# Kernel optimization log

Hardware: AMD Instinct MI355X
Metric: run time of the kernel (lower is better)

Reference implementation:

```python
import jax, jax.numpy as jnp
import numpy as np

INPUT_SIZE = 512
HIDDEN_SIZE = 256
B, S = 8, 2048


def setup_inputs() -> dict:
    key = jax.random.key(0)
    ks = jax.random.split(key, 9)
    d = INPUT_SIZE
    q = jax.random.normal(ks[0], (B, S, 2 * HIDDEN_SIZE), dtype=jnp.float32)
    k = jax.random.normal(ks[1], (B, S, d), dtype=jnp.float32)
    v = jax.random.normal(ks[2], (B, S, d), dtype=jnp.float32)
    # Params: module uses nn.init.normal_ (std=1); keep normal but scale for stability.
    Wq = jax.random.normal(ks[3], (2 * HIDDEN_SIZE, d), dtype=jnp.float32) * 0.02
    bq = jax.random.normal(ks[4], (d,), dtype=jnp.float32) * 0.02
    Wk = jax.random.normal(ks[5], (d, d), dtype=jnp.float32) * 0.02
    bk = jax.random.normal(ks[6], (d,), dtype=jnp.float32) * 0.02
    Wv = jax.random.normal(ks[7], (d, d), dtype=jnp.float32) * 0.02
    bv = jax.random.normal(ks[8], (d,), dtype=jnp.float32) * 0.02
    return {"q": q, "k": k, "v": v, "Wq": Wq, "bq": bq, "Wk": Wk, "bk": bk, "Wv": Wv, "bv": bv}


def reference(q, k, v, Wq, bq, Wk, bk, Wv, bv):
    d = Wq.shape[-1]
    qp = jnp.einsum('bsh,hd->bsd', q, Wq) + bq  # [B,S,d]
    kp = jnp.einsum('bse,ed->bsd', k, Wk) + bk
    vp = jnp.einsum('bse,ed->bsd', v, Wv) + bv
    scale = 1.0 / jnp.sqrt(jnp.float32(d))
    scores = jnp.einsum('bqd,bkd->bqk', qp, kp) * scale  # [B,S,S]
    attn = jax.nn.softmax(scores, axis=-1)
    return jnp.einsum('bqk,bkd->bqd', attn, vp)
```

## Files before the change

### kernel.cpp

```cpp
#include <hip/hip_runtime.h>
#include <hip/hip_bf16.h>
#include <stdint.h>


typedef __attribute__((ext_vector_type(8))) short short8;
typedef __attribute__((ext_vector_type(4))) float floatx4;

__device__ __forceinline__ unsigned short f2bf(float f) {
    union { float f; uint32_t u; } v; v.f = f;
    uint32_t u = v.u;
    return (unsigned short)((u + 0x7FFF + ((u >> 16) & 1)) >> 16);
}

#define ASYNC16(g, l)                                                          \
    __builtin_amdgcn_global_load_lds(                                          \
        (const __attribute__((address_space(1))) unsigned int*)(g),            \
        (__attribute__((address_space(3))) unsigned int*)(l), 16, 0, 0)

__global__ void wt_kernel(const float* __restrict__ Wq, const float* __restrict__ Wk,
                          const float* __restrict__ Wv, unsigned short* __restrict__ WT) {
    __shared__ float t[64][65];
    const int z = blockIdx.z;
    const float* W = (z == 0) ? Wq : ((z == 1) ? Wk : Wv);
    const int n0 = blockIdx.x * 64, k0 = blockIdx.y * 64;
    const int tx = threadIdx.x & 63, ty = threadIdx.x >> 6;
#pragma unroll
    for (int i = ty; i < 64; i += 4) t[i][tx] = W[(size_t)(k0 + i) * 512 + n0 + tx];
    __syncthreads();
#pragma unroll
    for (int i = ty; i < 64; i += 4)
        WT[(size_t)z * 262144 + (size_t)(n0 + i) * 512 + k0 + tx] = f2bf(t[tx][i]);
}

__global__ __launch_bounds__(256, 4) void proj_kernel(
    const float* __restrict__ q, const float* __restrict__ k, const float* __restrict__ v,
    const float* __restrict__ bq, const float* __restrict__ bk, const float* __restrict__ bv,
    const unsigned short* __restrict__ WT,
    unsigned short* __restrict__ qp, unsigned short* __restrict__ kp,
    unsigned short* __restrict__ vpT)
{
    __shared__ __align__(16) unsigned short At[2][64][32];
    __shared__ __align__(16) unsigned short Bt[2][256][32];

    const int z = blockIdx.z;
    const int tid = threadIdx.x;
    const int lane = tid & 63;
    const int wave = tid >> 6;
    const int col = lane & 15;
    const int quad = lane >> 4;

    const float* A = (z == 0) ? q : ((z == 1) ? k : v);
    const float* bias = (z == 0) ? bq : ((z == 1) ? bk : bv);
    const unsigned short* W = WT + (size_t)z * 262144;

    const int m0 = blockIdx.x * 64;
    const int n0b = blockIdx.y * 256;

    floatx4 acc[4][4];
#pragma unroll
    for (int mf = 0; mf < 4; ++mf)
#pragma unroll
        for (int nf = 0; nf < 4; ++nf) acc[mf][nf] = floatx4{0.f, 0.f, 0.f, 0.f};

    auto stageB = [&](int nb, int kc) {
#pragma unroll
        for (int j = 0; j < 4; ++j) {
            const int rr = (wave * 4 + j) * 16 + (lane >> 2);
            const unsigned short* g =
                W + (size_t)(n0b + rr) * 512 + kc * 32 + (((lane & 3) ^ ((rr >> 1) & 3)) << 3);
            ASYNC16(g, &Bt[nb][(wave * 4 + j) * 16][0]);
        }
    };

    float4 fA0, fA1;
    const int arow = tid >> 2;
    auto loadA = [&](int kc) {
        const float* ap = A + (size_t)(m0 + arow) * 512 + kc * 32 + (tid & 3) * 8;
        fA0 = *(const float4*)ap;
        fA1 = *(const float4*)(ap + 4);
    };
    auto writeA = [&](int nb) {
        short8 t;
        t[0] = f2bf(fA0.x); t[1] = f2bf(fA0.y); t[2] = f2bf(fA0.z); t[3] = f2bf(fA0.w);
        t[4] = f2bf(fA1.x); t[5] = f2bf(fA1.y); t[6] = f2bf(fA1.z); t[7] = f2bf(fA1.w);
        *(short8*)&At[nb][arow][(((tid & 3) ^ ((arow >> 1) & 3)) << 3)] = t;
    };

    stageB(0, 0);
    loadA(0);
    writeA(0);
    for (int kc = 0; kc < 16; ++kc) {
        const int cur = kc & 1;
        __syncthreads();
        if (kc < 15) { stageB(cur ^ 1, kc + 1); loadA(kc + 1); }

        const int rsw = (quad ^ ((col >> 1) & 3)) << 3;
        short8 a[4], bfr[4];
#pragma unroll
        for (int mf = 0; mf < 4; ++mf)
            a[mf] = *(const short8*)&At[cur][mf * 16 + col][rsw];
#pragma unroll
        for (int nf = 0; nf < 4; ++nf)
            bfr[nf] = *(const short8*)&Bt[cur][wave * 64 + nf * 16 + col][rsw];
#pragma unroll
        for (int mf = 0; mf < 4; ++mf)
#pragma unroll
            for (int nf = 0; nf < 4; ++nf)
                acc[mf][nf] = __builtin_amdgcn_mfma_f32_16x16x32_bf16(a[mf], bfr[nf], acc[mf][nf], 0, 0, 0);

        if (kc < 15) writeA(cur ^ 1);
    }

    const float scale = (z == 0) ? 0.04419417382415922f : 1.0f;
#pragma unroll
    for (int mf = 0; mf < 4; ++mf) {
#pragma unroll
        for (int nf = 0; nf < 4; ++nf) {
            const int n = n0b + wave * 64 + nf * 16 + col;
            const float bn2 = bias[n];
            floatx4 c = acc[mf][nf];
            if (z < 2) {
                unsigned short* outp = (z == 0) ? qp : kp;
#pragma unroll
                for (int r = 0; r < 4; ++r) {
                    int row = m0 + mf * 16 + quad * 4 + r;
                    outp[(size_t)row * 512 + n] = f2bf((c[r] + bn2) * scale);
                }
            } else {
                int row = m0 + mf * 16 + quad * 4;
                int bb = row >> 11;
                int s = row & 2047;
                ushort4 pk;
                pk.x = f2bf(c[0] + bn2); pk.y = f2bf(c[1] + bn2);
                pk.z = f2bf(c[2] + bn2); pk.w = f2bf(c[3] + bn2);
                *(ushort4*)(vpT + (((size_t)bb * 64 + (s >> 5)) * 512 + n) * 32 + (s & 31)) = pk;
            }
        }
    }
}

__global__ __launch_bounds__(512, 2) void attn_kernel(
    const unsigned short* __restrict__ qp, const unsigned short* __restrict__ kp,
    const unsigned short* __restrict__ vpT, float* __restrict__ out,
    float* __restrict__ Opart, float* __restrict__ lws)
{
    __shared__ __align__(16) unsigned short Kt[2][32][512];
    __shared__ __align__(16) unsigned short Vt[2][512][32];
    __shared__ __align__(16) unsigned short Pbuf[8][16][40];

    const int lane = threadIdx.x & 63;
    const int wave = threadIdx.x >> 6;
    const int col = lane & 15;
    const int quad = lane >> 4;
    const int b = blockIdx.x & 7;
    const int qt = (blockIdx.x >> 3) & 15;
    const int ksp = blockIdx.x >> 7;
    const int q0 = qt * 128 + wave * 16;
    const size_t rowbase = (size_t)b * 2048 + q0;

    const unsigned short* kpb = kp + (size_t)b * 2048 * 512;
    const unsigned short* vpb = vpT + ((size_t)b << 20);

    short8 aq[16];
#pragma unroll
    for (int kk = 0; kk < 16; ++kk)
        aq[kk] = *(const short8*)(qp + (rowbase + col) * 512 + kk * 32 + quad * 8);

    floatx4 o[32];
#pragma unroll
    for (int i = 0; i < 32; ++i) o[i] = floatx4{0.f, 0.f, 0.f, 0.f};
    float plsum[4] = {0.f, 0.f, 0.f, 0.f};

    auto stage = [&](int nb, int keyblk) {
#pragma unroll
        for (int j = 0; j < 4; ++j) {
            const int r = wave * 4 + j;
            const unsigned short* g =
                kpb + ((size_t)(keyblk * 32 + r) << 9) + ((lane ^ (r & 7)) << 3);
            ASYNC16(g, &Kt[nb][r][0]);
        }
        const unsigned short* vtile = vpb + ((size_t)keyblk << 14);
#pragma unroll
        for (int jj = 0; jj < 4; ++jj) {
            const int j2 = wave * 4 + jj;
            const int d = j2 * 16 + (lane >> 2);
            const unsigned short* g =
                vtile + ((size_t)d << 5) + (((lane & 3) ^ ((d >> 1) & 3)) << 3);
            ASYNC16(g, &Vt[nb][j2 * 16][0]);
        }
    };

    stage(0, ksp * 32);
    for (int kb = 0; kb < 32; ++kb) {
        const int cur = kb & 1;
        __syncthreads();
        if (kb < 31) stage(cur ^ 1, ksp * 32 + kb + 1);

        floatx4 s0 = floatx4{0.f, 0.f, 0.f, 0.f};
        floatx4 s1 = floatx4{0.f, 0.f, 0.f, 0.f};
        __builtin_amdgcn_s_setprio(1);
#pragma unroll
        for (int kk = 0; kk < 16; ++kk) {
            const int c = (kk << 2) + quad;
            short8 b0 = *(const short8*)&Kt[cur][col][(c ^ (col & 7)) << 3];
            short8 b1 = *(const short8*)&Kt[cur][16 + col][(c ^ (col & 7)) << 3];
            s0 = __builtin_amdgcn_mfma_f32_16x16x32_bf16(aq[kk], b0, s0, 0, 0, 0);
            s1 = __builtin_amdgcn_mfma_f32_16x16x32_bf16(aq[kk], b1, s1, 0, 0, 0);
        }
        __builtin_amdgcn_s_setprio(0);

#pragma unroll
        for (int r = 0; r < 4; ++r) {
            const float p0 = __expf(s0[r]);
            const float p1 = __expf(s1[r]);
            plsum[r] += p0 + p1;
            Pbuf[wave][quad * 4 + r][col]      = f2bf(p0);
            Pbuf[wave][quad * 4 + r][16 + col] = f2bf(p1);
        }
        const short8 aP = *(const short8*)&Pbuf[wave][col][quad * 8];

        __builtin_amdgcn_s_setprio(1);
#pragma unroll
        for (int nf = 0; nf < 32; ++nf) {
            const int d = nf * 16 + col;
            short8 bvf = *(const short8*)&Vt[cur][d][(quad ^ ((d >> 1) & 3)) << 3];
            o[nf] = __builtin_amdgcn_mfma_f32_16x16x32_bf16(aP, bvf, o[nf], 0, 0, 0);
        }
        __builtin_amdgcn_s_setprio(0);
    }

    float l[4];
#pragma unroll
    for (int r = 0; r < 4; ++r) {
        float acc_s = plsum[r];
#pragma unroll
        for (int off = 1; off <= 8; off <<= 1)
            acc_s += __shfl_xor(acc_s, off, 64);
        l[r] = acc_s;
    }
    float* obuf = (ksp == 0) ? out : Opart;
#pragma unroll
    for (int nf = 0; nf < 32; ++nf) {
#pragma unroll
        for (int r = 0; r < 4; ++r) {
            obuf[(rowbase + quad * 4 + r) * 512 + nf * 16 + col] = o[nf][r];
        }
    }
    if (col == 0) {
        float* lp = lws + ksp * 16384 + (int)rowbase;
#pragma unroll
        for (int r = 0; r < 4; ++r) lp[quad * 4 + r] = l[r];
    }
}

__global__ __launch_bounds__(256) void norm_kernel(float* __restrict__ out,
                                                   const float* __restrict__ Opart,
                                                   const float* __restrict__ lws)
{
    const size_t gid = (size_t)blockIdx.x * 256 + threadIdx.x;
    const int row = (int)(gid >> 7);
    const float rl = 1.0f / (lws[row] + lws[16384 + row]);
    float4 a = ((const float4*)out)[gid];
    float4 c = ((const float4*)Opart)[gid];
    float4 r;
    r.x = (a.x + c.x) * rl; r.y = (a.y + c.y) * rl;
    r.z = (a.z + c.z) * rl; r.w = (a.w + c.w) * rl;
    ((float4*)out)[gid] = r;
}

extern "C" void kernel_launch(void* const* d_in, const int* in_sizes, int n_in,
                              void* d_out, int out_size, void* d_ws, size_t ws_size,
                              hipStream_t stream) {
    const float* q  = (const float*)d_in[0];
    const float* k  = (const float*)d_in[1];
    const float* v  = (const float*)d_in[2];
    const float* Wq = (const float*)d_in[3];
    const float* bq = (const float*)d_in[4];
    const float* Wk = (const float*)d_in[5];
    const float* bk = (const float*)d_in[6];
    const float* Wv = (const float*)d_in[7];
    const float* bv = (const float*)d_in[8];
    float* out = (float*)d_out;

    unsigned short* WT  = (unsigned short*)d_ws;
    unsigned short* qp  = WT + (size_t)3 * 262144;
    unsigned short* kp  = qp + (size_t)16384 * 512;
    unsigned short* vpT = kp + (size_t)16384 * 512;
    float* Opart = (float*)(vpT + (size_t)16384 * 512);
    float* lws   = Opart + (size_t)8 * 2048 * 512;

    wt_kernel<<<dim3(8, 8, 3), 256, 0, stream>>>(Wq, Wk, Wv, WT);
    proj_kernel<<<dim3(256, 2, 3), 256, 0, stream>>>(q, k, v, bq, bk, bv, WT, qp, kp, vpT);
    attn_kernel<<<256, 512, 0, stream>>>(qp, kp, vpT, out, Opart, lws);
    norm_kernel<<<8192, 256, 0, stream>>>(out, Opart, lws);
}
```

Baseline: 315.1 us.

## Use 1024-thread attention blocks with a four-way key split

Adds a new attention kernel that uses 16 waves per block, with each block covering 256 query rows, and splits the key dimension four ways instead of two, keeping 256 blocks in total. Each K/V tile staged into shared memory is now reused by twice as many query waves, which cuts global/L2 traffic for K and V. The normalization kernel is generalized to sum any number of partial outputs. The cost is more partial-output traffic (three extra fp32 buffers written and read back) and one 1024-thread block per CU with heavy register use. The old path is kept as a fallback when the workspace is too small.

```diff
diff --git a/kernel.cpp b/kernel.cpp
--- a/kernel.cpp
+++ b/kernel.cpp
@@ -139,7 +139,121 @@
     }
 }
 
-__global__ __launch_bounds__(512, 2) void attn_kernel(
+__global__ __launch_bounds__(1024) void attn_kernel(
+    const unsigned short* __restrict__ qp, const unsigned short* __restrict__ kp,
+    const unsigned short* __restrict__ vpT, float* __restrict__ out,
+    float* __restrict__ Opart, float* __restrict__ lws)
+{
+    __shared__ __align__(16) unsigned short Kt[2][32][512];
+    __shared__ __align__(16) unsigned short Vt[2][512][32];
+    __shared__ __align__(16) unsigned short Pbuf[16][16][40];
+
+    const int lane = threadIdx.x & 63;
+    const int wave = threadIdx.x >> 6;
+    const int col = lane & 15;
+    const int quad = lane >> 4;
+    const int b = blockIdx.x & 7;
+    const int qt = (blockIdx.x >> 3) & 7;
+    const int ksp = blockIdx.x >> 6;
+    const int q0 = qt * 256 + wave * 16;
+    const size_t rowbase = (size_t)b * 2048 + q0;
+
+    const unsigned short* kpb = kp + (size_t)b * 2048 * 512;
+    const unsigned short* vpb = vpT + ((size_t)b << 20);
+
+    short8 aq[16];
+#pragma unroll
+    for (int kk = 0; kk < 16; ++kk)
+        aq[kk] = *(const short8*)(qp + (rowbase + col) * 512 + kk * 32 + quad * 8);
+
+    floatx4 o[32];
+#pragma unroll
+    for (int i = 0; i < 32; ++i) o[i] = floatx4{0.f, 0.f, 0.f, 0.f};
+    float plsum[4] = {0.f, 0.f, 0.f, 0.f};
+
+    auto stage = [&](int nb, int keyblk) {
+#pragma unroll
+        for (int j = 0; j < 2; ++j) {
+            const int r = wave * 2 + j;
+            const unsigned short* g =
+                kpb + ((size_t)(keyblk * 32 + r) << 9) + ((lane ^ (r & 7)) << 3);
+            ASYNC16(g, &Kt[nb][r][0]);
+        }
+        const unsigned short* vtile = vpb + ((size_t)keyblk << 14);
+#pragma unroll
+        for (int jj = 0; jj < 2; ++jj) {
+            const int j2 = wave * 2 + jj;
+            const int d = j2 * 16 + (lane >> 2);
+            const unsigned short* g =
+                vtile + ((size_t)d << 5) + (((lane & 3) ^ ((d >> 1) & 3)) << 3);
+            ASYNC16(g, &Vt[nb][j2 * 16][0]);
+        }
+    };
+
+    stage(0, ksp * 16);
+    for (int kb = 0; kb < 16; ++kb) {
+        const int cur = kb & 1;
+        __syncthreads();
+        if (kb < 15) stage(cur ^ 1, ksp * 16 + kb + 1);
+
+        floatx4 s0 = floatx4{0.f, 0.f, 0.f, 0.f};
+        floatx4 s1 = floatx4{0.f, 0.f, 0.f, 0.f};
+        __builtin_amdgcn_s_setprio(1);
+#pragma unroll
+        for (int kk = 0; kk < 16; ++kk) {
+            const int c = (kk << 2) + quad;
+            short8 b0 = *(const short8*)&Kt[cur][col][(c ^ (col & 7)) << 3];
+            short8 b1 = *(const short8*)&Kt[cur][16 + col][(c ^ (col & 7)) << 3];
+            s0 = __builtin_amdgcn_mfma_f32_16x16x32_bf16(aq[kk], b0, s0, 0, 0, 0);
+            s1 = __builtin_amdgcn_mfma_f32_16x16x32_bf16(aq[kk], b1, s1, 0, 0, 0);
+        }
+        __builtin_amdgcn_s_setprio(0);
+
+#pragma unroll
+        for (int r = 0; r < 4; ++r) {
+            const float p0 = __expf(s0[r]);
+            const float p1 = __expf(s1[r]);
+            plsum[r] += p0 + p1;
+            Pbuf[wave][quad * 4 + r][col]      = f2bf(p0);
+            Pbuf[wave][quad * 4 + r][16 + col] = f2bf(p1);
+        }
+        const short8 aP = *(const short8*)&Pbuf[wave][col][quad * 8];
+
+        __builtin_amdgcn_s_setprio(1);
+#pragma unroll
+        for (int nf = 0; nf < 32; ++nf) {
+            const int d = nf * 16 + col;
+            short8 bvf = *(const short8*)&Vt[cur][d][(quad ^ ((d >> 1) & 3)) << 3];
+            o[nf] = __builtin_amdgcn_mfma_f32_16x16x32_bf16(aP, bvf, o[nf], 0, 0, 0);
+        }
+        __builtin_amdgcn_s_setprio(0);
+    }
+
+    float l[4];
+#pragma unroll
+    for (int r = 0; r < 4; ++r) {
+        float acc_s = plsum[r];
+#pragma unroll
+        for (int off = 1; off <= 8; off <<= 1)
+            acc_s += __shfl_xor(acc_s, off, 64);
+        l[r] = acc_s;
+    }
+    float* obuf = (ksp == 0) ? out : (Opart + (size_t)(ksp - 1) * 8388608);
+#pragma unroll
+    for (int nf = 0; nf < 32; ++nf) {
+#pragma unroll
+        for (int r = 0; r < 4; ++r) {
+            obuf[(rowbase + quad * 4 + r) * 512 + nf * 16 + col] = o[nf][r];
+        }
+    }
+    if (col == 0) {
+        float* lp = lws + ksp * 16384 + (int)rowbase;
+#pragma unroll
+        for (int r = 0; r < 4; ++r) lp[quad * 4 + r] = l[r];
+    }
+}
+
+__global__ __launch_bounds__(512, 2) void attn_kernel_f(
     const unsigned short* __restrict__ qp, const unsigned short* __restrict__ kp,
     const unsigned short* __restrict__ vpT, float* __restrict__ out,
     float* __restrict__ Opart, float* __restrict__ lws)
@@ -255,16 +369,21 @@
 
 __global__ __launch_bounds__(256) void norm_kernel(float* __restrict__ out,
                                                    const float* __restrict__ Opart,
-                                                   const float* __restrict__ lws)
+                                                   const float* __restrict__ lws,
+                                                   int nsplit)
 {
     const size_t gid = (size_t)blockIdx.x * 256 + threadIdx.x;
     const int row = (int)(gid >> 7);
-    const float rl = 1.0f / (lws[row] + lws[16384 + row]);
+    float lsum = lws[row];
+    for (int s = 1; s < nsplit; ++s) lsum += lws[(size_t)s * 16384 + row];
+    const float rl = 1.0f / lsum;
     float4 a = ((const float4*)out)[gid];
-    float4 c = ((const float4*)Opart)[gid];
+    for (int s = 1; s < nsplit; ++s) {
+        float4 c = ((const float4*)Opart)[(size_t)(s - 1) * 2097152 + gid];
+        a.x += c.x; a.y += c.y; a.z += c.z; a.w += c.w;
+    }
     float4 r;
-    r.x = (a.x + c.x) * rl; r.y = (a.y + c.y) * rl;
-    r.z = (a.z + c.z) * rl; r.w = (a.w + c.w) * rl;
+    r.x = a.x * rl; r.y = a.y * rl; r.z = a.z * rl; r.w = a.w * rl;
     ((float4*)out)[gid] = r;
 }
 
@@ -287,10 +406,19 @@
     unsigned short* kp  = qp + (size_t)16384 * 512;
     unsigned short* vpT = kp + (size_t)16384 * 512;
     float* Opart = (float*)(vpT + (size_t)16384 * 512);
-    float* lws   = Opart + (size_t)8 * 2048 * 512;
+    const size_t need_big =
+        (size_t)3 * 262144 * 2 + (size_t)3 * 16384 * 512 * 2 +
+        (size_t)3 * 8388608 * 4 + (size_t)4 * 16384 * 4;
 
     wt_kernel<<<dim3(8, 8, 3), 256, 0, stream>>>(Wq, Wk, Wv, WT);
     proj_kernel<<<dim3(256, 2, 3), 256, 0, stream>>>(q, k, v, bq, bk, bv, WT, qp, kp, vpT);
-    attn_kernel<<<256, 512, 0, stream>>>(qp, kp, vpT, out, Opart, lws);
-    norm_kernel<<<8192, 256, 0, stream>>>(out, Opart, lws);
-}
+    if (ws_size >= need_big) {
+        float* lws = Opart + (size_t)3 * 8388608;
+        attn_kernel<<<256, 1024, 0, stream>>>(qp, kp, vpT, out, Opart, lws);
+        norm_kernel<<<8192, 256, 0, stream>>>(out, Opart, lws, 4);
+    } else {
+        float* lws = Opart + (size_t)1 * 8388608;
+        attn_kernel_f<<<256, 512, 0, stream>>>(qp, kp, vpT, out, Opart, lws);
+        norm_kernel<<<8192, 256, 0, stream>>>(out, Opart, lws, 2);
+    }
+}
```

Measured after the change: 711.2 us. +125.7%, slower.
